# Kernel optimization log

Measured on AMD Instinct MI355X. Metric: run time of the kernel, lower is better.

Reference implementation:

```python
import jax, jax.numpy as jnp
import numpy as np

N = 8192          # num nodes
F_IN = 512        # num_features
H = 256           # hidden_dim
D = 64            # embedding_dim
E = 262144        # num edges (avg degree 32)


def setup_inputs() -> dict:
    key = jax.random.key(0)
    ks = jax.random.split(key, 6)
    x = jax.random.normal(ks[0], (N, F_IN), dtype=jnp.float32)
    adj_rows = jax.random.randint(ks[1], (E,), 0, N)
    adj_cols = jax.random.randint(ks[2], (E,), 0, N)
    adj_vals = jax.random.uniform(ks[3], (E,), dtype=jnp.float32)
    W1 = jax.random.normal(ks[4], (F_IN, H), dtype=jnp.float32) / np.sqrt(F_IN)
    b1 = jnp.zeros((H,), dtype=jnp.float32)
    W2 = jax.random.normal(ks[5], (H, D), dtype=jnp.float32) / np.sqrt(H)
    b2 = jnp.zeros((D,), dtype=jnp.float32)
    return {"x": x, "adj_rows": adj_rows, "adj_cols": adj_cols,
            "adj_vals": adj_vals, "W1": W1, "b1": b1, "W2": W2, "b2": b2}


def _spmm(rows, cols, vals, dense):
    # sparse [N,N] @ dense [N,F] via gather + segment-sum (COO spmm)
    gathered = vals[:, None] * dense[cols]           # [E, F]
    return jax.ops.segment_sum(gathered, rows, num_segments=N)


def reference(x, adj_rows, adj_cols, adj_vals, W1, b1, W2, b2):
    # GCN layer 1: linear -> spmm -> relu (dropout is identity in eval mode)
    h = _spmm(adj_rows, adj_cols, adj_vals, x @ W1 + b1)   # [N, H]
    h = jax.nn.relu(h)
    # GCN layer 2: linear -> spmm
    z = _spmm(adj_rows, adj_cols, adj_vals, h @ W2 + b2)   # [N, D]
    # decode: sigmoid(z z^T)
    adj_rec = jax.nn.sigmoid(z @ z.T)                       # [N, N]
    return (z, adj_rec)
```

## Files before the change

### kernel.cpp

```cpp
#include <hip/hip_runtime.h>
#include <hip/hip_bf16.h>

#define NN 8192
#define FIN 512
#define HD 256
#define DD 64
#define NE 262144
#define BCAP 128

typedef __bf16 bf16_t;
typedef __bf16 bf16x8 __attribute__((ext_vector_type(8)));
typedef __bf16 bf16x4 __attribute__((ext_vector_type(4)));
typedef float f32x4 __attribute__((ext_vector_type(4)));

__global__ __launch_bounds__(256) void prep_kernel(const float* __restrict__ x, bf16_t* __restrict__ x_b,
                                                   const float* __restrict__ W1, bf16_t* __restrict__ w1t,
                                                   const float* __restrict__ W2, bf16_t* __restrict__ w2t,
                                                   int* __restrict__ deg) {
    int b = blockIdx.x;
    if (b < 4096) {
        int i = (b * 256 + threadIdx.x) * 4;
        float4 v = *reinterpret_cast<const float4*>(x + i);
        x_b[i + 0] = (bf16_t)v.x;
        x_b[i + 1] = (bf16_t)v.y;
        x_b[i + 2] = (bf16_t)v.z;
        x_b[i + 3] = (bf16_t)v.w;
    } else if (b < 4096 + 512) {
        int o = (b - 4096) * 256 + threadIdx.x;
        int r = o & 511;
        int c = o >> 9;
        w1t[o] = (bf16_t)W1[r * HD + c];
    } else if (b < 4096 + 512 + 64) {
        int o = (b - 4096 - 512) * 256 + threadIdx.x;
        int r = o & 255;
        int c = o >> 8;
        w2t[o] = (bf16_t)W2[r * DD + c];
    } else {
        int o = (b - 4096 - 512 - 64) * 256 + threadIdx.x;
        deg[o] = 0;
    }
}


__global__ void scatter_edges(const int* __restrict__ rows, const int* __restrict__ cols,
                              const float* __restrict__ vals,
                              int* __restrict__ deg, int* __restrict__ scol, float* __restrict__ sval) {
    int e = blockIdx.x * blockDim.x + threadIdx.x;
    if (e < NE) {
        int r = rows[e];
        int p = atomicAdd(&deg[r], 1);
        scol[r * BCAP + p] = cols[e];
        sval[r * BCAP + p] = vals[e];
    }
}


__global__ __launch_bounds__(256) void spmm_h_kernel(const int* __restrict__ deg,
                                                     const int* __restrict__ scol,
                                                     const float* __restrict__ sval,
                                                     const bf16_t* __restrict__ h0,
                                                     bf16_t* __restrict__ h) {
    int r = blockIdx.x;
    int wv = threadIdx.x >> 6;
    int lane = threadIdx.x & 63;
    int nd = deg[r];
    int base = r * BCAP;
    float a0 = 0.f, a1 = 0.f, a2 = 0.f, a3 = 0.f;
#pragma unroll 2
    for (int e = wv; e < nd; e += 4) {
        int c = scol[base + e];
        float v = sval[base + e];
        bf16x4 hv = *reinterpret_cast<const bf16x4*>(h0 + (size_t)c * HD + lane * 4);
        a0 += v * (float)hv[0];
        a1 += v * (float)hv[1];
        a2 += v * (float)hv[2];
        a3 += v * (float)hv[3];
    }
    __shared__ float red[4][256];
    red[wv][lane * 4 + 0] = a0;
    red[wv][lane * 4 + 1] = a1;
    red[wv][lane * 4 + 2] = a2;
    red[wv][lane * 4 + 3] = a3;
    __syncthreads();
    if (wv == 0) {
#pragma unroll
        for (int j = 0; j < 4; j++) {
            int f = lane * 4 + j;
            float s = red[0][f] + red[1][f] + red[2][f] + red[3][f];
            h[(size_t)r * HD + f] = (bf16_t)fmaxf(s, 0.f);
        }
    }
}

__global__ __launch_bounds__(256) void spmm_z_kernel(const int* __restrict__ deg,
                                                     const int* __restrict__ scol,
                                                     const float* __restrict__ sval,
                                                     const bf16_t* __restrict__ z0,
                                                     float* __restrict__ z_out,
                                                     bf16_t* __restrict__ z_b) {
    int r = blockIdx.x * 4 + (threadIdx.x >> 6);
    int lane = threadIdx.x & 63;
    int nd = deg[r];
    int base = r * BCAP;
    float acc = 0.f;
#pragma unroll 4
    for (int e = 0; e < nd; e++)
        acc += sval[base + e] * (float)z0[(size_t)scol[base + e] * DD + lane];
    z_out[(size_t)r * DD + lane] = acc;
    z_b[(size_t)r * DD + lane] = (bf16_t)acc;
}

template <int ACT, typename OutT, int MW>
__global__ __launch_bounds__(256) void gemm_bt(const bf16_t* __restrict__ A,
                                               const bf16_t* __restrict__ Bt,
                                               const float* __restrict__ bias,
                                               OutT* __restrict__ C,
                                               int M, int N, int K) {
    int wave = threadIdx.x >> 6;
    int lane = threadIdx.x & 63;
    int lr = lane & 15;
    int lq = lane >> 4;
    int m0 = blockIdx.x * (64 * MW) + wave * (16 * MW);
    int n0 = blockIdx.y * 64;

    f32x4 acc[MW][4];
#pragma unroll
    for (int i = 0; i < MW; i++)
#pragma unroll
        for (int t = 0; t < 4; t++) acc[i][t] = {0.f, 0.f, 0.f, 0.f};

    const bf16_t* Abase = A + (size_t)(m0 + lr) * K + lq * 8;
    const bf16_t* Bbase = Bt + (size_t)(n0 + lr) * K + lq * 8;

    for (int k0 = 0; k0 < K; k0 += 32) {
        bf16x8 a[MW];
#pragma unroll
        for (int i = 0; i < MW; i++)
            a[i] = *reinterpret_cast<const bf16x8*>(Abase + (size_t)i * 16 * K + k0);
#pragma unroll
        for (int t = 0; t < 4; t++) {
            bf16x8 b = *reinterpret_cast<const bf16x8*>(Bbase + (size_t)t * 16 * K + k0);
#pragma unroll
            for (int i = 0; i < MW; i++)
                acc[i][t] = __builtin_amdgcn_mfma_f32_16x16x32_bf16(a[i], b, acc[i][t], 0, 0, 0);
        }
    }

    if (ACT == 2) {
        __shared__ float ldsT[256 / 64 * 16 * MW][65];
        int rbase = wave * 16 * MW;
#pragma unroll
        for (int i = 0; i < MW; i++)
#pragma unroll
            for (int t = 0; t < 4; t++)
#pragma unroll
                for (int r = 0; r < 4; r++) {
                    float v = acc[i][t][r];
                    v = 1.f / (1.f + __expf(-v));
                    ldsT[rbase + i * 16 + lq * 4 + r][t * 16 + lr] = v;
                }
        int c4 = (lane & 15) * 4;
        int rr = lane >> 4;
#pragma unroll
        for (int j = 0; j < 4 * MW; j++) {
            int row_l = rbase + j * 4 + rr;
            f32x4 v = *reinterpret_cast<const f32x4*>(&ldsT[row_l][c4]);
            size_t gaddr = (size_t)(blockIdx.x * (64 * MW) + row_l) * N + n0 + c4;
            *reinterpret_cast<f32x4*>(&C[gaddr]) = v;
        }
    } else {
#pragma unroll
        for (int i = 0; i < MW; i++) {
#pragma unroll
            for (int t = 0; t < 4; t++) {
                int col = n0 + t * 16 + lr;
                float bv = bias ? bias[col] : 0.f;
#pragma unroll
                for (int r = 0; r < 4; r++) {
                    int row = m0 + i * 16 + lq * 4 + r;
                    C[(size_t)row * N + col] = (OutT)(acc[i][t][r] + bv);
                }
            }
        }
    }
}


extern "C" void kernel_launch(void* const* d_in, const int* in_sizes, int n_in,
                              void* d_out, int out_size, void* d_ws, size_t ws_size,
                              hipStream_t stream) {
    const float* x   = (const float*)d_in[0];
    const int* rows  = (const int*)d_in[1];
    const int* cols  = (const int*)d_in[2];
    const float* vals = (const float*)d_in[3];
    const float* W1  = (const float*)d_in[4];
    const float* b1  = (const float*)d_in[5];
    const float* W2  = (const float*)d_in[6];
    const float* b2  = (const float*)d_in[7];

    float* out_z   = (float*)d_out;
    float* out_adj = out_z + (size_t)NN * DD;

    char* ws = (char*)d_ws;
    size_t off = 0;
    auto alloc = [&](size_t bytes) { void* p = ws + off; off += (bytes + 255) & ~(size_t)255; return p; };
    bf16_t* x_b   = (bf16_t*)alloc((size_t)NN * FIN * 2);
    bf16_t* w1t   = (bf16_t*)alloc((size_t)HD * FIN * 2);
    bf16_t* w2t   = (bf16_t*)alloc((size_t)DD * HD * 2);
    bf16_t* h0    = (bf16_t*)alloc((size_t)NN * HD * 2);
    bf16_t* h_b   = (bf16_t*)alloc((size_t)NN * HD * 2);
    bf16_t* z0    = (bf16_t*)alloc((size_t)NN * DD * 2);
    bf16_t* z_b   = (bf16_t*)alloc((size_t)NN * DD * 2);
    int* deg      = (int*)alloc((size_t)NN * 4);
    int* scol     = (int*)alloc((size_t)NN * BCAP * 4);
    float* sval   = (float*)alloc((size_t)NN * BCAP * 4);

    prep_kernel<<<4096 + 512 + 64 + 32, 256, 0, stream>>>(x, x_b, W1, w1t, W2, w2t, deg);

    scatter_edges<<<NE / 256, 256, 0, stream>>>(rows, cols, vals, deg, scol, sval);

    gemm_bt<0, bf16_t, 1><<<dim3(NN / 64, HD / 64), 256, 0, stream>>>(x_b, w1t, b1, h0, NN, HD, FIN);

    spmm_h_kernel<<<NN, 256, 0, stream>>>(deg, scol, sval, h0, h_b);

    gemm_bt<0, bf16_t, 1><<<dim3(NN / 64, DD / 64), 256, 0, stream>>>(h_b, w2t, b2, z0, NN, DD, HD);

    spmm_z_kernel<<<NN / 4, 256, 0, stream>>>(deg, scol, sval, z0, out_z, z_b);

    gemm_bt<2, float, 2><<<dim3(NN / 128, NN / 64), 256, 0, stream>>>(z_b, z_b, nullptr, out_adj, NN, NN, DD);
}
```

Measured before the change: 385.4 us.

## Widen spmm gathers, split spmm_z edges across lanes, swap decode grid order

```diff
diff --git a/kernel.cpp b/kernel.cpp
--- a/kernel.cpp
+++ b/kernel.cpp
@@ -63,32 +63,40 @@
     int r = blockIdx.x;
     int wv = threadIdx.x >> 6;
     int lane = threadIdx.x & 63;
+    int half = lane >> 5;
+    int fl = lane & 31;
     int nd = deg[r];
     int base = r * BCAP;
-    float a0 = 0.f, a1 = 0.f, a2 = 0.f, a3 = 0.f;
+    float a[8];
+#pragma unroll
+    for (int j = 0; j < 8; j++) a[j] = 0.f;
 #pragma unroll 2
-    for (int e = wv; e < nd; e += 4) {
+    for (int e = wv * 2 + half; e < nd; e += 8) {
         int c = scol[base + e];
         float v = sval[base + e];
-        bf16x4 hv = *reinterpret_cast<const bf16x4*>(h0 + (size_t)c * HD + lane * 4);
-        a0 += v * (float)hv[0];
-        a1 += v * (float)hv[1];
-        a2 += v * (float)hv[2];
-        a3 += v * (float)hv[3];
-    }
+        bf16x8 hv = *reinterpret_cast<const bf16x8*>(h0 + (size_t)c * HD + fl * 8);
+#pragma unroll
+        for (int j = 0; j < 8; j++) a[j] += v * (float)hv[j];
+    }
+#pragma unroll
+    for (int j = 0; j < 8; j++) a[j] += __shfl_xor(a[j], 32);
     __shared__ float red[4][256];
-    red[wv][lane * 4 + 0] = a0;
-    red[wv][lane * 4 + 1] = a1;
-    red[wv][lane * 4 + 2] = a2;
-    red[wv][lane * 4 + 3] = a3;
+    if (half == 0) {
+#pragma unroll
+        for (int j = 0; j < 8; j++) red[wv][fl * 8 + j] = a[j];
+    }
     __syncthreads();
     if (wv == 0) {
-#pragma unroll
-        for (int j = 0; j < 4; j++) {
-            int f = lane * 4 + j;
-            float s = red[0][f] + red[1][f] + red[2][f] + red[3][f];
-            h[(size_t)r * HD + f] = (bf16_t)fmaxf(s, 0.f);
-        }
+        f32x4 s = *reinterpret_cast<const f32x4*>(&red[0][lane * 4]);
+#pragma unroll
+        for (int p = 1; p < 4; p++) {
+            f32x4 t = *reinterpret_cast<const f32x4*>(&red[p][lane * 4]);
+            s += t;
+        }
+        bf16x4 o;
+#pragma unroll
+        for (int j = 0; j < 4; j++) o[j] = (bf16_t)fmaxf(s[j], 0.f);
+        *reinterpret_cast<bf16x4*>(h + (size_t)r * HD + lane * 4) = o;
     }
 }
 
@@ -100,14 +108,32 @@
                                                      bf16_t* __restrict__ z_b) {
     int r = blockIdx.x * 4 + (threadIdx.x >> 6);
     int lane = threadIdx.x & 63;
+    int sub = lane >> 4;
+    int fl = lane & 15;
     int nd = deg[r];
     int base = r * BCAP;
-    float acc = 0.f;
-#pragma unroll 4
-    for (int e = 0; e < nd; e++)
-        acc += sval[base + e] * (float)z0[(size_t)scol[base + e] * DD + lane];
-    z_out[(size_t)r * DD + lane] = acc;
-    z_b[(size_t)r * DD + lane] = (bf16_t)acc;
+    float a0 = 0.f, a1 = 0.f, a2 = 0.f, a3 = 0.f;
+#pragma unroll 2
+    for (int e = sub; e < nd; e += 4) {
+        int c = scol[base + e];
+        float v = sval[base + e];
+        bf16x4 zv = *reinterpret_cast<const bf16x4*>(z0 + (size_t)c * DD + fl * 4);
+        a0 += v * (float)zv[0];
+        a1 += v * (float)zv[1];
+        a2 += v * (float)zv[2];
+        a3 += v * (float)zv[3];
+    }
+    a0 += __shfl_xor(a0, 16); a0 += __shfl_xor(a0, 32);
+    a1 += __shfl_xor(a1, 16); a1 += __shfl_xor(a1, 32);
+    a2 += __shfl_xor(a2, 16); a2 += __shfl_xor(a2, 32);
+    a3 += __shfl_xor(a3, 16); a3 += __shfl_xor(a3, 32);
+    if (sub == 0) {
+        f32x4 o = {a0, a1, a2, a3};
+        *reinterpret_cast<f32x4*>(z_out + (size_t)r * DD + fl * 4) = o;
+        bf16x4 ob;
+        ob[0] = (bf16_t)a0; ob[1] = (bf16_t)a1; ob[2] = (bf16_t)a2; ob[3] = (bf16_t)a3;
+        *reinterpret_cast<bf16x4*>(z_b + (size_t)r * DD + fl * 4) = ob;
+    }
 }
 
 template <int ACT, typename OutT, int MW>
@@ -120,8 +146,11 @@
     int lane = threadIdx.x & 63;
     int lr = lane & 15;
     int lq = lane >> 4;
-    int m0 = blockIdx.x * (64 * MW) + wave * (16 * MW);
-    int n0 = blockIdx.y * 64;
+    int bm = (ACT == 2) ? blockIdx.y : blockIdx.x;
+    int bn = (ACT == 2) ? blockIdx.x : blockIdx.y;
+    int mblk = bm * (64 * MW);
+    int m0 = mblk + wave * (16 * MW);
+    int n0 = bn * 64;
 
     f32x4 acc[MW][4];
 #pragma unroll
@@ -165,7 +194,7 @@
         for (int j = 0; j < 4 * MW; j++) {
             int row_l = rbase + j * 4 + rr;
             f32x4 v = *reinterpret_cast<const f32x4*>(&ldsT[row_l][c4]);
-            size_t gaddr = (size_t)(blockIdx.x * (64 * MW) + row_l) * N + n0 + c4;
+            size_t gaddr = (size_t)(mblk + row_l) * N + n0 + c4;
             *reinterpret_cast<f32x4*>(&C[gaddr]) = v;
         }
     } else {
@@ -227,5 +256,5 @@
 
     spmm_z_kernel<<<NN / 4, 256, 0, stream>>>(deg, scol, sval, z0, out_z, z_b);
 
-    gemm_bt<2, float, 2><<<dim3(NN / 128, NN / 64), 256, 0, stream>>>(z_b, z_b, nullptr, out_adj, NN, NN, DD);
-}
+    gemm_bt<2, float, 2><<<dim3(NN / 64, NN / 128), 256, 0, stream>>>(z_b, z_b, nullptr, out_adj, NN, NN, DD);
+}
```

Result: faster. 376.3 us (-2.4%).
